# Performance work log

Measured on AMD Instinct MI355X. Metric: run time of the kernel, lower is better.

## Reference

```python
import jax, jax.numpy as jnp
import numpy as np

B, T = 16384, 128  # batch, n_frames


def setup_inputs() -> dict:
    key = jax.random.key(0)
    k0, k1, k2, k3, k4, k5 = jax.random.split(key, 6)
    dir = jax.random.normal(k0, (B, 3), dtype=jnp.float32)
    R = jax.random.normal(k1, (B, T, 3, 3), dtype=jnp.float32)
    s = 1.0 / np.sqrt(3.0)  # torch LSTM default init scale (uniform +-1/sqrt(hidden))
    W_ih = jax.random.uniform(k2, (12, 3), jnp.float32, -s, s)
    W_hh = jax.random.uniform(k3, (12, 3), jnp.float32, -s, s)
    b_ih = jax.random.uniform(k4, (12,), jnp.float32, -s, s)
    b_hh = jax.random.uniform(k5, (12,), jnp.float32, -s, s)
    return {"dir": dir, "R": R, "W_ih": W_ih, "W_hh": W_hh, "b_ih": b_ih, "b_hh": b_hh}


def _rot_step(v, Rm):
    # v: [B,3], Rm: [B,3,3] -> Rm @ v
    nv = jnp.einsum('bij,bj->bi', Rm, v)
    return nv, nv


def _build_dirs(dir, R):
    n_frames = R.shape[1]
    half = n_frames // 2
    # Backward chain: dirs[i] = R[half-1-i]^T @ ... @ R[half-1]^T @ dir
    Rt_back = jnp.swapaxes(jnp.flip(R[:, :half], axis=1), 2, 3)  # [B, half, 3, 3]
    _, back = jax.lax.scan(_rot_step, dir, jnp.swapaxes(Rt_back, 0, 1))  # [half, B, 3]
    # Forward chain: dirs[i] = R[i-1] @ ... @ R[half] @ dir for i in half+1..n-1
    Rf = jnp.swapaxes(R[:, half:n_frames - 1], 0, 1)  # [n-1-half, B, 3, 3]
    _, fwd = jax.lax.scan(_rot_step, dir, Rf)  # [n-1-half, B, 3]
    dirs_tm = jnp.concatenate([back, dir[None], fwd], axis=0)  # time-major [T, B, 3]
    return dirs_tm, half


def _lstm(dirs_tm, W_ih, W_hh, b_ih, b_hh):
    Bsz = dirs_tm.shape[1]
    h0 = jnp.zeros((Bsz, 3), dirs_tm.dtype)
    c0 = jnp.zeros((Bsz, 3), dirs_tm.dtype)
    bias = b_ih + b_hh

    def step(carry, x):
        h, c = carry
        gates = x @ W_ih.T + h @ W_hh.T + bias  # [B,12]
        i = jax.nn.sigmoid(gates[:, 0:3])
        f = jax.nn.sigmoid(gates[:, 3:6])
        g = jnp.tanh(gates[:, 6:9])
        o = jax.nn.sigmoid(gates[:, 9:12])
        c = f * c + i * g
        h = o * jnp.tanh(c)
        return (h, c), h

    _, h_seq = jax.lax.scan(step, (h0, c0), dirs_tm)  # [T, B, 3]
    return h_seq


def reference(dir, R, W_ih, W_hh, b_ih, b_hh):
    dirs_tm, half = _build_dirs(dir, R)
    h_seq = _lstm(dirs_tm, W_ih, W_hh, b_ih, b_hh)
    dirs_out = jnp.swapaxes(dirs_tm, 0, 1)  # [B, T, 3]
    return dirs_out.at[:, half, :].set(h_seq[half])
```

## Files before the change

kernel.cpp:

```cpp
#include <hip/hip_runtime.h>

typedef float f4 __attribute__((ext_vector_type(4)));
typedef float f4u __attribute__((ext_vector_type(4), aligned(4)));

struct M3 { float m[3][3]; };

#define ELEM(q, n) ((q)[(n) >> 2][(n) & 3])

__device__ __forceinline__ M3 matmul(const M3& A, const M3& B) {
  M3 C;
#pragma unroll
  for (int i = 0; i < 3; ++i)
#pragma unroll
    for (int j = 0; j < 3; ++j)
      C.m[i][j] = A.m[i][0]*B.m[0][j] + A.m[i][1]*B.m[1][j] + A.m[i][2]*B.m[2][j];
  return C;
}

__device__ __forceinline__ M3 shfl_mat(const M3& A, int srcLane) {
  M3 C;
#pragma unroll
  for (int i = 0; i < 3; ++i)
#pragma unroll
    for (int j = 0; j < 3; ++j)
      C.m[i][j] = __shfl(A.m[i][j], srcLane, 64);
  return C;
}

__device__ __forceinline__ M3 build_D(const f4 (&q)[9], int kf, int kb, bool tb) {
  M3 D;
#pragma unroll
  for (int i = 0; i < 3; ++i)
#pragma unroll
    for (int j = 0; j < 3; ++j) {
      float a = ELEM(q, 9*kf + 3*i + j);
      float c = ELEM(q, 9*kb + 3*j + i);
      D.m[i][j] = tb ? c : a;
    }
  return D;
}

__device__ __forceinline__ float sigm(float z) {
  return __builtin_amdgcn_rcpf(1.0f + __expf(-z));
}
__device__ __forceinline__ float tanh_(float z) {
  float e = __expf(2.0f * z);
  return 1.0f - 2.0f * __builtin_amdgcn_rcpf(e + 1.0f);
}

template <int CTRL>
__device__ __forceinline__ float quad_bcast(float v) {
  return __int_as_float(
      __builtin_amdgcn_mov_dpp(__float_as_int(v), CTRL, 0xf, 0xf, true));
}

#define EPB 16
#define XIDX(t, e) ((t)*17 + 2*((t) >> 3) + (e))

__global__ __launch_bounds__(256) void fused_kernel(
    const float* __restrict__ dir, const float* __restrict__ R,
    const float* __restrict__ Wih, const float* __restrict__ Whh,
    const float* __restrict__ bih, const float* __restrict__ bhh,
    float* __restrict__ out, int B) {
  __shared__ f4 xrows[64 * 17 + 2 * 7 + 16];

  const int tid = threadIdx.x;
  const int lane = tid & 63;
  const int l = tid & 15;
  const int s = l & 7;
  const bool tb = (l < 8);
  const bool skip = (!tb) && (s == 7);
  const int eloc = tid >> 4;
  const int b = blockIdx.x * EPB + eloc;
  const bool valid = (b < B);

  f4 qa[9], qb[9];
  float d0 = 0.f, d1 = 0.f, d2 = 0.f;
  if (valid) {
    const float* Rb = R + (size_t)b * 1152;
    const int lo = tb ? (56 - 8*s) : (64 + 8*s);
    const int gA = tb ? lo + 4 : lo;
    const int gB = tb ? lo : lo + 4;
    const f4* pA = (const f4*)(Rb + gA * 9);
    const f4* pB = (const f4*)(Rb + gB * 9);
#pragma unroll
    for (int i = 0; i < 9; ++i) { qa[i] = pA[i]; qb[i] = pB[i]; }
    d0 = dir[3*b+0]; d1 = dir[3*b+1]; d2 = dir[3*b+2];
  } else {
#pragma unroll
    for (int i = 0; i < 9; ++i) { qa[i] = (f4){0,0,0,0}; qb[i] = (f4){0,0,0,0}; }
  }

  M3 S = build_D(qa, 0, 3, tb);
#pragma unroll
  for (int j = 1; j < 4; ++j) S = matmul(build_D(qa, j, 3 - j, tb), S);
#pragma unroll
  for (int j = 0; j < 4; ++j) S = matmul(build_D(qb, j, 3 - j, tb), S);

  M3 I = S;
#pragma unroll
  for (int d = 1; d < 8; d <<= 1) {
    M3 Sh = shfl_mat(I, lane - d);
    M3 T = matmul(I, Sh);
#pragma unroll
    for (int i = 0; i < 3; ++i)
#pragma unroll
      for (int j = 0; j < 3; ++j)
        I.m[i][j] = (s >= d) ? T.m[i][j] : I.m[i][j];
  }

  float w0 = I.m[0][0]*d0 + I.m[0][1]*d1 + I.m[0][2]*d2;
  float w1 = I.m[1][0]*d0 + I.m[1][1]*d1 + I.m[1][2]*d2;
  float w2 = I.m[2][0]*d0 + I.m[2][1]*d1 + I.m[2][2]*d2;
  float p0 = __shfl(w0, lane - 1, 64);
  float p1 = __shfl(w1, lane - 1, 64);
  float p2 = __shfl(w2, lane - 1, 64);
  float v0 = (s == 0) ? d0 : p0;
  float v1 = (s == 0) ? d1 : p1;
  float v2 = (s == 0) ? d2 : p2;

  float row[24];
#pragma unroll
  for (int j = 0; j < 8; ++j) {
    M3 D = (j < 4) ? build_D(qa, j, 3 - j, tb) : build_D(qb, j - 4, 7 - j, tb);
    float n0 = D.m[0][0]*v0 + D.m[0][1]*v1 + D.m[0][2]*v2;
    float n1 = D.m[1][0]*v0 + D.m[1][1]*v1 + D.m[1][2]*v2;
    float n2 = D.m[2][0]*v0 + D.m[2][1]*v1 + D.m[2][2]*v2;
    v0 = n0; v1 = n1; v2 = n2;
    row[3*j+0] = n0; row[3*j+1] = n1; row[3*j+2] = n2;
  }

  if (valid) {
    float* obE = out + (size_t)b * 384;
    const int rowBase = tb ? 8*s : 65 + 8*s;
    float* ob = obE + (size_t)rowBase * 3;
#pragma unroll
    for (int kk = 0; kk < 5; ++kk) {
      f4u vv = { row[4*kk+0], row[4*kk+1], row[4*kk+2], row[4*kk+3] };
      *(f4u*)(ob + 4*kk) = vv;
    }
    ob[20] = row[20];
    if (!skip) { ob[21] = row[21]; ob[22] = row[22]; ob[23] = row[23]; }
  }

  if (tb) {
#pragma unroll
    for (int n = 0; n < 8; ++n) {
      f4 vv = { row[3*n+0], row[3*n+1], row[3*n+2], 0.f };
      xrows[XIDX(8*s + n, eloc)] = vv;
    }
  }

  __syncthreads();

  const int lstm_wave = blockIdx.x & 3;
  if ((tid >> 6) != lstm_wave) return;

  const int e2 = lane >> 2;
  const int u = lane & 3;
  const int uu = (u == 3) ? 0 : u;
  const int b2 = blockIdx.x * EPB + e2;
  const bool valid2 = (b2 < B);
  const int b2c = valid2 ? b2 : 0;

  const float wii0 = Wih[uu*3+0],     wii1 = Wih[uu*3+1],     wii2 = Wih[uu*3+2];
  const float wif0 = Wih[(3+uu)*3+0], wif1 = Wih[(3+uu)*3+1], wif2 = Wih[(3+uu)*3+2];
  const float wig0 = Wih[(6+uu)*3+0], wig1 = Wih[(6+uu)*3+1], wig2 = Wih[(6+uu)*3+2];
  const float wio0 = Wih[(9+uu)*3+0], wio1 = Wih[(9+uu)*3+1], wio2 = Wih[(9+uu)*3+2];
  const float whi0 = Whh[uu*3+0],     whi1 = Whh[uu*3+1],     whi2 = Whh[uu*3+2];
  const float whf0 = Whh[(3+uu)*3+0], whf1 = Whh[(3+uu)*3+1], whf2 = Whh[(3+uu)*3+2];
  const float whg0 = Whh[(6+uu)*3+0], whg1 = Whh[(6+uu)*3+1], whg2 = Whh[(6+uu)*3+2];
  const float who0 = Whh[(9+uu)*3+0], who1 = Whh[(9+uu)*3+1], who2 = Whh[(9+uu)*3+2];
  const float bsi = bih[uu]   + bhh[uu];
  const float bsf = bih[3+uu] + bhh[3+uu];
  const float bsg = bih[6+uu] + bhh[6+uu];
  const float bso = bih[9+uu] + bhh[9+uu];

  const float dd0 = dir[3*b2c+0], dd1 = dir[3*b2c+1], dd2 = dir[3*b2c+2];

  float h0 = 0.f, h1 = 0.f, h2 = 0.f, cc = 0.f, hl = 0.f;

#define LSTEP(x0_, x1_, x2_)                                                  \
  {                                                                           \
    float zi = bsi + wii0*(x0_) + wii1*(x1_) + wii2*(x2_)                     \
                   + whi0*h0 + whi1*h1 + whi2*h2;                             \
    float zf = bsf + wif0*(x0_) + wif1*(x1_) + wif2*(x2_)                     \
                   + whf0*h0 + whf1*h1 + whf2*h2;                             \
    float zg = bsg + wig0*(x0_) + wig1*(x1_) + wig2*(x2_)                     \
                   + whg0*h0 + whg1*h1 + whg2*h2;                             \
    float zo = bso + wio0*(x0_) + wio1*(x1_) + wio2*(x2_)                     \
                   + who0*h0 + who1*h1 + who2*h2;                             \
    float ai = sigm(zi), af = sigm(zf), ag = tanh_(zg), ao = sigm(zo);        \
    cc = af*cc + ai*ag;                                                       \
    float hn = ao * tanh_(cc);                                                \
    hl = hn;                                                                  \
    h0 = quad_bcast<0x00>(hn);                                                \
    h1 = quad_bcast<0x55>(hn);                                                \
    h2 = quad_bcast<0xAA>(hn);                                                \
  }

  f4 xa[8], xb[8];
#pragma unroll
  for (int j = 0; j < 8; ++j) xa[j] = xrows[XIDX(j, e2)];
#pragma unroll
  for (int c = 0; c < 8; ++c) {
    if (c < 7) {
      if ((c & 1) == 0) {
#pragma unroll
        for (int j = 0; j < 8; ++j) xb[j] = xrows[XIDX((c+1)*8 + j, e2)];
      } else {
#pragma unroll
        for (int j = 0; j < 8; ++j) xa[j] = xrows[XIDX((c+1)*8 + j, e2)];
      }
    }
#pragma unroll
    for (int j = 0; j < 8; ++j) {
      f4 x = ((c & 1) == 0) ? xa[j] : xb[j];
      LSTEP(x[0], x[1], x[2]);
    }
  }
  LSTEP(dd0, dd1, dd2);
#undef LSTEP

  if (valid2 && u < 3) out[(size_t)b2 * 384 + 192 + u] = hl;
}

extern "C" void kernel_launch(void* const* d_in, const int* in_sizes, int n_in,
                              void* d_out, int out_size, void* d_ws, size_t ws_size,
                              hipStream_t stream) {
  const float* dir = (const float*)d_in[0];
  const float* R   = (const float*)d_in[1];
  const float* Wih = (const float*)d_in[2];
  const float* Whh = (const float*)d_in[3];
  const float* bih = (const float*)d_in[4];
  const float* bhh = (const float*)d_in[5];
  float* out = (float*)d_out;

  const int B = in_sizes[0] / 3;
  const int grid = (B + EPB - 1) / EPB;
  hipLaunchKernelGGL(fused_kernel, dim3(grid), dim3(256), 0, stream,
                     dir, R, Wih, Whh, bih, bhh, out, B);
}
```

Measured before the change: 36.71 us.

## Split backward and forward chains into separate blocks with DPP prefix scans

Blocks are now specialised: half handle the backward rotation chain plus the LSTM for 32 elements, half handle the forward chain only, instead of each block doing both halves for 16 elements with divergent build_D selects. The cross-lane matrix prefix scan switches from __shfl to DPP row-shift moves, and the backward half works with untransposed matrices by reversing the multiplication order. The LSTM now runs on half-lanes of all four waves rather than one wave per block. Load balance between block types is uneven, since only backward blocks run the long serial LSTM.

```diff
diff --git a/kernel.cpp b/kernel.cpp
--- a/kernel.cpp
+++ b/kernel.cpp
@@ -17,27 +17,31 @@
   return C;
 }
 
-__device__ __forceinline__ M3 shfl_mat(const M3& A, int srcLane) {
+__device__ __forceinline__ M3 mk(const f4 (&q)[9], int k) {
+  M3 A;
+#pragma unroll
+  for (int i = 0; i < 3; ++i)
+#pragma unroll
+    for (int j = 0; j < 3; ++j)
+      A.m[i][j] = ELEM(q, 9*k + 3*i + j);
+  return A;
+}
+
+template <int CTRL>
+__device__ __forceinline__ float dppf(float v) {
+  return __int_as_float(
+      __builtin_amdgcn_mov_dpp(__float_as_int(v), CTRL, 0xf, 0xf, true));
+}
+
+template <int D>
+__device__ __forceinline__ M3 dpp_shr_mat(const M3& A) {
   M3 C;
 #pragma unroll
   for (int i = 0; i < 3; ++i)
 #pragma unroll
     for (int j = 0; j < 3; ++j)
-      C.m[i][j] = __shfl(A.m[i][j], srcLane, 64);
+      C.m[i][j] = dppf<0x110 + D>(A.m[i][j]);
   return C;
-}
-
-__device__ __forceinline__ M3 build_D(const f4 (&q)[9], int kf, int kb, bool tb) {
-  M3 D;
-#pragma unroll
-  for (int i = 0; i < 3; ++i)
-#pragma unroll
-    for (int j = 0; j < 3; ++j) {
-      float a = ELEM(q, 9*kf + 3*i + j);
-      float c = ELEM(q, 9*kb + 3*j + i);
-      D.m[i][j] = tb ? c : a;
-    }
-  return D;
 }
 
 __device__ __forceinline__ float sigm(float z) {
@@ -54,131 +58,119 @@
       __builtin_amdgcn_mov_dpp(__float_as_int(v), CTRL, 0xf, 0xf, true));
 }
 
-#define EPB 16
-#define XIDX(t, e) ((t)*17 + 2*((t) >> 3) + (e))
-
-__global__ __launch_bounds__(256) void fused_kernel(
+__global__ __launch_bounds__(256, 4) void fused_kernel(
     const float* __restrict__ dir, const float* __restrict__ R,
     const float* __restrict__ Wih, const float* __restrict__ Whh,
     const float* __restrict__ bih, const float* __restrict__ bhh,
-    float* __restrict__ out, int B) {
-  __shared__ f4 xrows[64 * 17 + 2 * 7 + 16];
+    float* __restrict__ out, int B, int nbBack) {
+  __shared__ f4 xrows[64 * 33];
 
   const int tid = threadIdx.x;
-  const int lane = tid & 63;
-  const int l = tid & 15;
-  const int s = l & 7;
-  const bool tb = (l < 8);
-  const bool skip = (!tb) && (s == 7);
-  const int eloc = tid >> 4;
-  const int b = blockIdx.x * EPB + eloc;
-  const bool valid = (b < B);
-
-  f4 qa[9], qb[9];
-  float d0 = 0.f, d1 = 0.f, d2 = 0.f;
-  if (valid) {
-    const float* Rb = R + (size_t)b * 1152;
-    const int lo = tb ? (56 - 8*s) : (64 + 8*s);
-    const int gA = tb ? lo + 4 : lo;
-    const int gB = tb ? lo : lo + 4;
-    const f4* pA = (const f4*)(Rb + gA * 9);
-    const f4* pB = (const f4*)(Rb + gB * 9);
-#pragma unroll
-    for (int i = 0; i < 9; ++i) { qa[i] = pA[i]; qb[i] = pB[i]; }
-    d0 = dir[3*b+0]; d1 = dir[3*b+1]; d2 = dir[3*b+2];
-  } else {
-#pragma unroll
-    for (int i = 0; i < 9; ++i) { qa[i] = (f4){0,0,0,0}; qb[i] = (f4){0,0,0,0}; }
-  }
-
-  M3 S = build_D(qa, 0, 3, tb);
-#pragma unroll
-  for (int j = 1; j < 4; ++j) S = matmul(build_D(qa, j, 3 - j, tb), S);
-#pragma unroll
-  for (int j = 0; j < 4; ++j) S = matmul(build_D(qb, j, 3 - j, tb), S);
-
-  M3 I = S;
-#pragma unroll
-  for (int d = 1; d < 8; d <<= 1) {
-    M3 Sh = shfl_mat(I, lane - d);
-    M3 T = matmul(I, Sh);
-#pragma unroll
-    for (int i = 0; i < 3; ++i)
-#pragma unroll
-      for (int j = 0; j < 3; ++j)
-        I.m[i][j] = (s >= d) ? T.m[i][j] : I.m[i][j];
-  }
-
-  float w0 = I.m[0][0]*d0 + I.m[0][1]*d1 + I.m[0][2]*d2;
-  float w1 = I.m[1][0]*d0 + I.m[1][1]*d1 + I.m[1][2]*d2;
-  float w2 = I.m[2][0]*d0 + I.m[2][1]*d1 + I.m[2][2]*d2;
-  float p0 = __shfl(w0, lane - 1, 64);
-  float p1 = __shfl(w1, lane - 1, 64);
-  float p2 = __shfl(w2, lane - 1, 64);
-  float v0 = (s == 0) ? d0 : p0;
-  float v1 = (s == 0) ? d1 : p1;
-  float v2 = (s == 0) ? d2 : p2;
-
-  float row[24];
-#pragma unroll
-  for (int j = 0; j < 8; ++j) {
-    M3 D = (j < 4) ? build_D(qa, j, 3 - j, tb) : build_D(qb, j - 4, 7 - j, tb);
-    float n0 = D.m[0][0]*v0 + D.m[0][1]*v1 + D.m[0][2]*v2;
-    float n1 = D.m[1][0]*v0 + D.m[1][1]*v1 + D.m[1][2]*v2;
-    float n2 = D.m[2][0]*v0 + D.m[2][1]*v1 + D.m[2][2]*v2;
-    v0 = n0; v1 = n1; v2 = n2;
-    row[3*j+0] = n0; row[3*j+1] = n1; row[3*j+2] = n2;
-  }
-
-  if (valid) {
-    float* obE = out + (size_t)b * 384;
-    const int rowBase = tb ? 8*s : 65 + 8*s;
-    float* ob = obE + (size_t)rowBase * 3;
-#pragma unroll
-    for (int kk = 0; kk < 5; ++kk) {
-      f4u vv = { row[4*kk+0], row[4*kk+1], row[4*kk+2], row[4*kk+3] };
-      *(f4u*)(ob + 4*kk) = vv;
-    }
-    ob[20] = row[20];
-    if (!skip) { ob[21] = row[21]; ob[22] = row[22]; ob[23] = row[23]; }
-  }
-
-  if (tb) {
-#pragma unroll
-    for (int n = 0; n < 8; ++n) {
-      f4 vv = { row[3*n+0], row[3*n+1], row[3*n+2], 0.f };
-      xrows[XIDX(8*s + n, eloc)] = vv;
-    }
-  }
-
-  __syncthreads();
-
-  const int lstm_wave = blockIdx.x & 3;
-  if ((tid >> 6) != lstm_wave) return;
-
-  const int e2 = lane >> 2;
-  const int u = lane & 3;
-  const int uu = (u == 3) ? 0 : u;
-  const int b2 = blockIdx.x * EPB + e2;
-  const bool valid2 = (b2 < B);
-  const int b2c = valid2 ? b2 : 0;
-
-  const float wii0 = Wih[uu*3+0],     wii1 = Wih[uu*3+1],     wii2 = Wih[uu*3+2];
-  const float wif0 = Wih[(3+uu)*3+0], wif1 = Wih[(3+uu)*3+1], wif2 = Wih[(3+uu)*3+2];
-  const float wig0 = Wih[(6+uu)*3+0], wig1 = Wih[(6+uu)*3+1], wig2 = Wih[(6+uu)*3+2];
-  const float wio0 = Wih[(9+uu)*3+0], wio1 = Wih[(9+uu)*3+1], wio2 = Wih[(9+uu)*3+2];
-  const float whi0 = Whh[uu*3+0],     whi1 = Whh[uu*3+1],     whi2 = Whh[uu*3+2];
-  const float whf0 = Whh[(3+uu)*3+0], whf1 = Whh[(3+uu)*3+1], whf2 = Whh[(3+uu)*3+2];
-  const float whg0 = Whh[(6+uu)*3+0], whg1 = Whh[(6+uu)*3+1], whg2 = Whh[(6+uu)*3+2];
-  const float who0 = Whh[(9+uu)*3+0], who1 = Whh[(9+uu)*3+1], who2 = Whh[(9+uu)*3+2];
-  const float bsi = bih[uu]   + bhh[uu];
-  const float bsf = bih[3+uu] + bhh[3+uu];
-  const float bsg = bih[6+uu] + bhh[6+uu];
-  const float bso = bih[9+uu] + bhh[9+uu];
-
-  const float dd0 = dir[3*b2c+0], dd1 = dir[3*b2c+1], dd2 = dir[3*b2c+2];
-
-  float h0 = 0.f, h1 = 0.f, h2 = 0.f, cc = 0.f, hl = 0.f;
+  const int e = tid >> 3;
+  const int s = tid & 7;
+
+  if ((int)blockIdx.x < nbBack) {
+    const int b = blockIdx.x * 32 + e;
+    const bool valid = (b < B);
+    const int bc = valid ? b : 0;
+    const float* Rb = R + (size_t)bc * 1152;
+    const int lo = 56 - 8 * s;
+
+    f4 qa[9], qb[9];
+    {
+      const f4* pA = (const f4*)(Rb + lo * 9);
+      const f4* pB = (const f4*)(Rb + (lo + 4) * 9);
+#pragma unroll
+      for (int i = 0; i < 9; ++i) { qa[i] = pA[i]; qb[i] = pB[i]; }
+    }
+    const float d0 = dir[3*bc+0], d1 = dir[3*bc+1], d2 = dir[3*bc+2];
+
+    M3 P = mk(qa, 0);
+#pragma unroll
+    for (int k = 1; k < 4; ++k) P = matmul(mk(qa, k), P);
+#pragma unroll
+    for (int k = 0; k < 4; ++k) P = matmul(mk(qb, k), P);
+
+    M3 I = P;
+    {
+      M3 Sh = dpp_shr_mat<1>(I); M3 T = matmul(Sh, I);
+#pragma unroll
+      for (int i = 0; i < 3; ++i)
+#pragma unroll
+        for (int j = 0; j < 3; ++j) I.m[i][j] = (s >= 1) ? T.m[i][j] : I.m[i][j];
+    }
+    {
+      M3 Sh = dpp_shr_mat<2>(I); M3 T = matmul(Sh, I);
+#pragma unroll
+      for (int i = 0; i < 3; ++i)
+#pragma unroll
+        for (int j = 0; j < 3; ++j) I.m[i][j] = (s >= 2) ? T.m[i][j] : I.m[i][j];
+    }
+    {
+      M3 Sh = dpp_shr_mat<4>(I); M3 T = matmul(Sh, I);
+#pragma unroll
+      for (int i = 0; i < 3; ++i)
+#pragma unroll
+        for (int j = 0; j < 3; ++j) I.m[i][j] = (s >= 4) ? T.m[i][j] : I.m[i][j];
+    }
+
+    float w0 = I.m[0][0]*d0 + I.m[1][0]*d1 + I.m[2][0]*d2;
+    float w1 = I.m[0][1]*d0 + I.m[1][1]*d1 + I.m[2][1]*d2;
+    float w2 = I.m[0][2]*d0 + I.m[1][2]*d1 + I.m[2][2]*d2;
+    float p0 = dppf<0x111>(w0), p1 = dppf<0x111>(w1), p2 = dppf<0x111>(w2);
+    float v0 = (s == 0) ? d0 : p0;
+    float v1 = (s == 0) ? d1 : p1;
+    float v2 = (s == 0) ? d2 : p2;
+
+    float row[24];
+#pragma unroll
+    for (int j = 0; j < 8; ++j) {
+      M3 A = (j < 4) ? mk(qb, 3 - j) : mk(qa, 7 - j);
+      float n0 = v0*A.m[0][0] + v1*A.m[1][0] + v2*A.m[2][0];
+      float n1 = v0*A.m[0][1] + v1*A.m[1][1] + v2*A.m[2][1];
+      float n2 = v0*A.m[0][2] + v1*A.m[1][2] + v2*A.m[2][2];
+      v0 = n0; v1 = n1; v2 = n2;
+      row[3*j+0] = n0; row[3*j+1] = n1; row[3*j+2] = n2;
+    }
+
+    if (valid) {
+      float* ob = out + (size_t)b * 384 + 24 * s;
+#pragma unroll
+      for (int kk = 0; kk < 6; ++kk) {
+        f4 vv = { row[4*kk+0], row[4*kk+1], row[4*kk+2], row[4*kk+3] };
+        ((f4u*)ob)[kk] = vv;
+      }
+    }
+#pragma unroll
+    for (int j = 0; j < 8; ++j) {
+      f4 vv = { row[3*j+0], row[3*j+1], row[3*j+2], 0.f };
+      xrows[(8*s + j) * 33 + e] = vv;
+    }
+
+    __syncthreads();
+
+    const int wv = tid >> 6, ln = tid & 63;
+    if (ln >= 32) return;
+    const int e2 = wv * 8 + (ln >> 2);
+    const int u = ln & 3, uu = (u == 3) ? 0 : u;
+    const int b2 = blockIdx.x * 32 + e2;
+    if (b2 >= B) return;
+
+    const float wii0 = Wih[uu*3+0],     wii1 = Wih[uu*3+1],     wii2 = Wih[uu*3+2];
+    const float wif0 = Wih[(3+uu)*3+0], wif1 = Wih[(3+uu)*3+1], wif2 = Wih[(3+uu)*3+2];
+    const float wig0 = Wih[(6+uu)*3+0], wig1 = Wih[(6+uu)*3+1], wig2 = Wih[(6+uu)*3+2];
+    const float wio0 = Wih[(9+uu)*3+0], wio1 = Wih[(9+uu)*3+1], wio2 = Wih[(9+uu)*3+2];
+    const float whi0 = Whh[uu*3+0],     whi1 = Whh[uu*3+1],     whi2 = Whh[uu*3+2];
+    const float whf0 = Whh[(3+uu)*3+0], whf1 = Whh[(3+uu)*3+1], whf2 = Whh[(3+uu)*3+2];
+    const float whg0 = Whh[(6+uu)*3+0], whg1 = Whh[(6+uu)*3+1], whg2 = Whh[(6+uu)*3+2];
+    const float who0 = Whh[(9+uu)*3+0], who1 = Whh[(9+uu)*3+1], who2 = Whh[(9+uu)*3+2];
+    const float bsi = bih[uu]   + bhh[uu];
+    const float bsf = bih[3+uu] + bhh[3+uu];
+    const float bsg = bih[6+uu] + bhh[6+uu];
+    const float bso = bih[9+uu] + bhh[9+uu];
+    const float dd0 = dir[3*b2+0], dd1 = dir[3*b2+1], dd2 = dir[3*b2+2];
+
+    float h0 = 0.f, h1 = 0.f, h2 = 0.f, cc = 0.f, hl = 0.f;
 
 #define LSTEP(x0_, x1_, x2_)                                                  \
   {                                                                           \
@@ -199,30 +191,106 @@
     h2 = quad_bcast<0xAA>(hn);                                                \
   }
 
-  f4 xa[8], xb[8];
-#pragma unroll
-  for (int j = 0; j < 8; ++j) xa[j] = xrows[XIDX(j, e2)];
-#pragma unroll
-  for (int c = 0; c < 8; ++c) {
-    if (c < 7) {
-      if ((c & 1) == 0) {
-#pragma unroll
-        for (int j = 0; j < 8; ++j) xb[j] = xrows[XIDX((c+1)*8 + j, e2)];
-      } else {
-#pragma unroll
-        for (int j = 0; j < 8; ++j) xa[j] = xrows[XIDX((c+1)*8 + j, e2)];
+    f4 xa[8], xb[8];
+#pragma unroll
+    for (int j = 0; j < 8; ++j) xa[j] = xrows[j * 33 + e2];
+#pragma unroll
+    for (int c = 0; c < 8; ++c) {
+      if (c < 7) {
+        if ((c & 1) == 0) {
+#pragma unroll
+          for (int j = 0; j < 8; ++j) xb[j] = xrows[((c+1)*8 + j) * 33 + e2];
+        } else {
+#pragma unroll
+          for (int j = 0; j < 8; ++j) xa[j] = xrows[((c+1)*8 + j) * 33 + e2];
+        }
       }
-    }
+#pragma unroll
+      for (int j = 0; j < 8; ++j) {
+        f4 x = ((c & 1) == 0) ? xa[j] : xb[j];
+        LSTEP(x[0], x[1], x[2]);
+      }
+    }
+    LSTEP(dd0, dd1, dd2);
+#undef LSTEP
+
+    if (u < 3) out[(size_t)b2 * 384 + 192 + u] = hl;
+
+  } else {
+    const int b = ((int)blockIdx.x - nbBack) * 32 + e;
+    const bool valid = (b < B);
+    const int bc = valid ? b : 0;
+    const float* Rb = R + (size_t)bc * 1152;
+    const int lo = 64 + 8 * s;
+
+    f4 qa[9], qb[9];
+    {
+      const f4* pA = (const f4*)(Rb + lo * 9);
+      const f4* pB = (const f4*)(Rb + (lo + 4) * 9);
+#pragma unroll
+      for (int i = 0; i < 9; ++i) { qa[i] = pA[i]; qb[i] = pB[i]; }
+    }
+    const float d0 = dir[3*bc+0], d1 = dir[3*bc+1], d2 = dir[3*bc+2];
+
+    M3 P = mk(qa, 0);
+#pragma unroll
+    for (int k = 1; k < 4; ++k) P = matmul(mk(qa, k), P);
+#pragma unroll
+    for (int k = 0; k < 4; ++k) P = matmul(mk(qb, k), P);
+
+    M3 I = P;
+    {
+      M3 Sh = dpp_shr_mat<1>(I); M3 T = matmul(I, Sh);
+#pragma unroll
+      for (int i = 0; i < 3; ++i)
+#pragma unroll
+        for (int j = 0; j < 3; ++j) I.m[i][j] = (s >= 1) ? T.m[i][j] : I.m[i][j];
+    }
+    {
+      M3 Sh = dpp_shr_mat<2>(I); M3 T = matmul(I, Sh);
+#pragma unroll
+      for (int i = 0; i < 3; ++i)
+#pragma unroll
+        for (int j = 0; j < 3; ++j) I.m[i][j] = (s >= 2) ? T.m[i][j] : I.m[i][j];
+    }
+    {
+      M3 Sh = dpp_shr_mat<4>(I); M3 T = matmul(I, Sh);
+#pragma unroll
+      for (int i = 0; i < 3; ++i)
+#pragma unroll
+        for (int j = 0; j < 3; ++j) I.m[i][j] = (s >= 4) ? T.m[i][j] : I.m[i][j];
+    }
+
+    float w0 = I.m[0][0]*d0 + I.m[0][1]*d1 + I.m[0][2]*d2;
+    float w1 = I.m[1][0]*d0 + I.m[1][1]*d1 + I.m[1][2]*d2;
+    float w2 = I.m[2][0]*d0 + I.m[2][1]*d1 + I.m[2][2]*d2;
+    float p0 = dppf<0x111>(w0), p1 = dppf<0x111>(w1), p2 = dppf<0x111>(w2);
+    float v0 = (s == 0) ? d0 : p0;
+    float v1 = (s == 0) ? d1 : p1;
+    float v2 = (s == 0) ? d2 : p2;
+
+    float row[24];
 #pragma unroll
     for (int j = 0; j < 8; ++j) {
-      f4 x = ((c & 1) == 0) ? xa[j] : xb[j];
-      LSTEP(x[0], x[1], x[2]);
+      M3 A = (j < 4) ? mk(qa, j) : mk(qb, j - 4);
+      float n0 = A.m[0][0]*v0 + A.m[0][1]*v1 + A.m[0][2]*v2;
+      float n1 = A.m[1][0]*v0 + A.m[1][1]*v1 + A.m[1][2]*v2;
+      float n2 = A.m[2][0]*v0 + A.m[2][1]*v1 + A.m[2][2]*v2;
+      v0 = n0; v1 = n1; v2 = n2;
+      row[3*j+0] = n0; row[3*j+1] = n1; row[3*j+2] = n2;
+    }
+
+    if (valid) {
+      float* ob = out + (size_t)b * 384 + (size_t)(65 + 8*s) * 3;
+#pragma unroll
+      for (int kk = 0; kk < 5; ++kk) {
+        f4u vv = { row[4*kk+0], row[4*kk+1], row[4*kk+2], row[4*kk+3] };
+        *(f4u*)(ob + 4*kk) = vv;
+      }
+      ob[20] = row[20];
+      if (s < 7) { ob[21] = row[21]; ob[22] = row[22]; ob[23] = row[23]; }
     }
   }
-  LSTEP(dd0, dd1, dd2);
-#undef LSTEP
-
-  if (valid2 && u < 3) out[(size_t)b2 * 384 + 192 + u] = hl;
 }
 
 extern "C" void kernel_launch(void* const* d_in, const int* in_sizes, int n_in,
@@ -237,7 +305,8 @@
   float* out = (float*)d_out;
 
   const int B = in_sizes[0] / 3;
-  const int grid = (B + EPB - 1) / EPB;
+  const int nbBack = (B + 31) / 32;
+  const int grid = nbBack * 2;
   hipLaunchKernelGGL(fused_kernel, dim3(grid), dim3(256), 0, stream,
-                     dir, R, Wih, Whh, bih, bhh, out, B);
-}
+                     dir, R, Wih, Whh, bih, bhh, out, B, nbBack);
+}
```

Measured after the change: 35.77 us. 1.03x faster.
